# Kernel tuning notes

Hardware: AMD Instinct MI355X
Metric: run time of the kernel (lower is better)

The kernel has to match this reference:

```python
import jax, jax.numpy as jnp
import numpy as np

NUM_NODES = 100000
NUM_EDGES = 1600000
IN_DIM = 128
HID = 128
OUT_DIM = 5


def setup_inputs() -> dict:
    key = jax.random.key(0)
    ks = jax.random.split(key, 8)
    x = jax.random.normal(ks[0], (NUM_NODES, IN_DIM), dtype=jnp.float32)
    edges = jax.random.randint(ks[1], (2, NUM_EDGES), 0, NUM_NODES, dtype=jnp.int32)
    s = 1.0 / np.sqrt(IN_DIM)
    W1 = jax.random.uniform(ks[2], (IN_DIM, HID), jnp.float32, -s, s)
    b1 = jax.random.uniform(ks[3], (HID,), jnp.float32, -s, s)
    sh = 1.0 / np.sqrt(HID)
    W2 = jax.random.uniform(ks[4], (HID, HID), jnp.float32, -sh, sh)
    b2 = jax.random.uniform(ks[5], (HID,), jnp.float32, -sh, sh)
    Wp = jax.random.uniform(ks[6], (HID, OUT_DIM), jnp.float32, -sh, sh)
    bp = jax.random.uniform(ks[7], (OUT_DIM,), jnp.float32, -sh, sh)
    return {"x": x, "edges": edges, "W1": W1, "b1": b1, "W2": W2, "b2": b2, "Wp": Wp, "bp": bp}


def _gnn_layer(x, src, tgt, W, b):
    # scatter-add of source features into targets (mean aggregation)
    agg = jax.ops.segment_sum(x[src], tgt, num_segments=NUM_NODES)  # [N, d]
    cnt = jax.ops.segment_sum(jnp.ones_like(tgt, dtype=x.dtype), tgt, num_segments=NUM_NODES)
    cnt = jnp.maximum(cnt, 1.0)  # clamp(min=1)
    agg = agg / cnt[:, None]
    combined = x + agg  # residual
    return jax.nn.relu(combined @ W + b)


def reference(x, edges, W1, b1, W2, b2, Wp, bp):
    src, tgt = edges[0], edges[1]
    h = _gnn_layer(x, src, tgt, W1, b1)
    h = _gnn_layer(h, src, tgt, W2, b2)
    return h @ Wp + bp  # [N, OUT_DIM]
```

## Files before the change

### kernel.cpp

```cpp
#include <hip/hip_runtime.h>

typedef unsigned int uint32;
typedef unsigned short ushort16;

typedef __attribute__((ext_vector_type(8))) short short8;
typedef __attribute__((ext_vector_type(4))) float f32x4;


#define RSH 9
#define NRG 512
#define CAP 12288
#define CH  2048

__device__ __forceinline__ ushort16 f2bf(float f) {
    uint32 u = __float_as_uint(f);
    u += 0x7fffu + ((u >> 16) & 1u);
    return (ushort16)(u >> 16);
}
__device__ __forceinline__ float bfhi(uint32 u) { return __uint_as_float(u & 0xffff0000u); }
__device__ __forceinline__ float bflo(uint32 u) { return __uint_as_float(u << 16); }
__device__ __forceinline__ uint32 pack2(float a, float b) {
    return (uint32)f2bf(a) | ((uint32)f2bf(b) << 16);
}

union U16 { uint4 u; short8 s; };
__device__ __forceinline__ short8 ld_frag(const ushort16* p) {
    U16 x; x.u = *(const uint4*)p; return x.s;
}

#define ACC8(v) \
    acc[0] += bflo(v.x); acc[1] += bfhi(v.x); \
    acc[2] += bflo(v.y); acc[3] += bfhi(v.y); \
    acc[4] += bflo(v.z); acc[5] += bfhi(v.z); \
    acc[6] += bflo(v.w); acc[7] += bfhi(v.w);

__global__ __launch_bounds__(256)
void count_prep_kernel(const int* __restrict__ tgt, int* __restrict__ hist,
                       const float* __restrict__ W1, const float* __restrict__ W2,
                       ushort16* __restrict__ Wt1, ushort16* __restrict__ Wt2,
                       int E, int PB) {
    int tid = threadIdx.x, blk = blockIdx.x;
    if (blk >= PB) {
        int idx = blk - PB;
        const float* W = (idx >> 3) ? W2 : W1;
        ushort16* Wt = (idx >> 3) ? Wt2 : Wt1;
        int i0 = (idx & 7) * 2048 + tid * 8;
        float4 a = *(const float4*)(W + i0);
        float4 b = *(const float4*)(W + i0 + 4);
        int k = i0 >> 7, col = i0 & 127;
        Wt[(col + 0) * 128 + k] = f2bf(a.x);
        Wt[(col + 1) * 128 + k] = f2bf(a.y);
        Wt[(col + 2) * 128 + k] = f2bf(a.z);
        Wt[(col + 3) * 128 + k] = f2bf(a.w);
        Wt[(col + 4) * 128 + k] = f2bf(b.x);
        Wt[(col + 5) * 128 + k] = f2bf(b.y);
        Wt[(col + 6) * 128 + k] = f2bf(b.z);
        Wt[(col + 7) * 128 + k] = f2bf(b.w);
        return;
    }
    __shared__ int cnt[256];
    cnt[tid] = 0;
    __syncthreads();
    int q0 = blk * (CH / 4), q1 = min(q0 + CH / 4, E / 4);
    for (int q = q0 + tid; q < q1; q += 256) {
        int4 t = ((const int4*)tgt)[q];
        atomicAdd(&cnt[t.x >> RSH], 1);
        atomicAdd(&cnt[t.y >> RSH], 1);
        atomicAdd(&cnt[t.z >> RSH], 1);
        atomicAdd(&cnt[t.w >> RSH], 1);
    }
    if (blk == 0 && tid == 0)
        for (int e = (E / 4) * 4; e < E; ++e) atomicAdd(&cnt[tgt[e] >> RSH], 1);
    __syncthreads();
    hist[(size_t)blk * 256 + tid] = cnt[tid];
}

__global__ __launch_bounds__(256)
void scan_kernel(int* __restrict__ hist, int* __restrict__ total, int PB) {
    __shared__ int sd[256];
    __shared__ int carrySh;
    int r = blockIdx.x, tid = threadIdx.x;
    if (tid == 0) carrySh = 0;
    __syncthreads();
    int chunks = (PB + 255) >> 8;
    for (int ch = 0; ch < chunks; ++ch) {
        int g = ch * 256 + tid;
        int v = (g < PB) ? hist[(size_t)g * 256 + r] : 0;
        int c0 = carrySh;
        sd[tid] = v;
        __syncthreads();
        for (int o = 1; o < 256; o <<= 1) {
            int t = (tid >= o) ? sd[tid - o] : 0;
            __syncthreads();
            sd[tid] += t;
            __syncthreads();
        }
        if (g < PB) hist[(size_t)g * 256 + r] = sd[tid] - v + c0;
        int tot = sd[255];
        __syncthreads();
        if (tid == 0) carrySh = c0 + tot;
        __syncthreads();
    }
    if (tid == 0) total[r] = carrySh;
}

__global__ __launch_bounds__(256)
void scatter_kernel(const int* __restrict__ src, const int* __restrict__ tgt,
                    const int* __restrict__ hist, uint2* __restrict__ rlist,
                    int E) {
    __shared__ int cb[256];
    __shared__ int cnt[256];
    int tid = threadIdx.x, blk = blockIdx.x;
    cnt[tid] = 0;
    cb[tid] = hist[(size_t)blk * 256 + tid];
    __syncthreads();
    int q0 = blk * (CH / 4), q1 = min(q0 + CH / 4, E / 4);
    for (int q = q0 + tid; q < q1; q += 256) {
        int4 t = ((const int4*)tgt)[q];
        int4 s = ((const int4*)src)[q];
        int r0 = t.x >> RSH, r1 = t.y >> RSH, r2 = t.z >> RSH, r3 = t.w >> RSH;
        int p0 = cb[r0] + atomicAdd(&cnt[r0], 1);
        int p1 = cb[r1] + atomicAdd(&cnt[r1], 1);
        int p2 = cb[r2] + atomicAdd(&cnt[r2], 1);
        int p3 = cb[r3] + atomicAdd(&cnt[r3], 1);
        if (p0 < CAP) rlist[(size_t)r0 * CAP + p0] = make_uint2((uint32)s.x, (uint32)t.x);
        if (p1 < CAP) rlist[(size_t)r1 * CAP + p1] = make_uint2((uint32)s.y, (uint32)t.y);
        if (p2 < CAP) rlist[(size_t)r2 * CAP + p2] = make_uint2((uint32)s.z, (uint32)t.z);
        if (p3 < CAP) rlist[(size_t)r3 * CAP + p3] = make_uint2((uint32)s.w, (uint32)t.w);
    }
    if (blk == 0 && tid == 0) {
        for (int e = (E / 4) * 4; e < E; ++e) {
            int t = tgt[e], r = t >> RSH;
            int p = cb[r] + atomicAdd(&cnt[r], 1);
            if (p < CAP) rlist[(size_t)r * CAP + p] = make_uint2((uint32)src[e], (uint32)t);
        }
    }
}

__global__ __launch_bounds__(512)
void csr_cvt_kernel(const uint2* __restrict__ rlist, const int* __restrict__ total,
                    int* __restrict__ start, int* __restrict__ deg,
                    int* __restrict__ csr, int N, int R, int CVB,
                    const float* __restrict__ x, uint4* __restrict__ xb) {
    int blk = blockIdx.x;
    int tid = threadIdx.x;
    if (blk >= R) {
        int n16 = N * 16;
        for (int j = (blk - R) * 512 + tid; j < n16; j += CVB * 512) {
            const float* p = x + (size_t)j * 8;
            float4 a = *(const float4*)p;
            float4 b = *(const float4*)(p + 4);
            uint4 o;
            o.x = pack2(a.x, a.y); o.y = pack2(a.z, a.w);
            o.z = pack2(b.x, b.y); o.w = pack2(b.z, b.w);
            xb[j] = o;
        }
        return;
    }
    __shared__ int lhist[NRG];
    __shared__ int sd[512];
    __shared__ int rbaseSh, countSh;

    int r = blk;
    if (tid < 256) sd[tid] = (tid < R) ? total[tid] : 0;
    __syncthreads();
    for (int o = 1; o < 256; o <<= 1) {
        int t = (tid >= o && tid < 256) ? sd[tid - o] : 0;
        __syncthreads();
        if (tid < 256) sd[tid] += t;
        __syncthreads();
    }
    if (tid == 0) {
        rbaseSh = (r == 0) ? 0 : sd[r - 1];
        countSh = min(total[r], CAP);
    }
    if (tid < NRG) lhist[tid] = 0;
    __syncthreads();
    int count = countSh;
    const uint2* rl = rlist + (size_t)r * CAP;
    int n0 = r << RSH;

    {
        int i = tid;
        for (; i + 512 * 7 < count; i += 512 * 8) {
            uint2 e0 = rl[i], e1 = rl[i + 512], e2 = rl[i + 1024], e3 = rl[i + 1536];
            uint2 e4 = rl[i + 2048], e5 = rl[i + 2560], e6 = rl[i + 3072], e7 = rl[i + 3584];
            atomicAdd(&lhist[e0.y & (NRG - 1)], 1);
            atomicAdd(&lhist[e1.y & (NRG - 1)], 1);
            atomicAdd(&lhist[e2.y & (NRG - 1)], 1);
            atomicAdd(&lhist[e3.y & (NRG - 1)], 1);
            atomicAdd(&lhist[e4.y & (NRG - 1)], 1);
            atomicAdd(&lhist[e5.y & (NRG - 1)], 1);
            atomicAdd(&lhist[e6.y & (NRG - 1)], 1);
            atomicAdd(&lhist[e7.y & (NRG - 1)], 1);
        }
        for (; i < count; i += 512)
            atomicAdd(&lhist[rl[i].y & (NRG - 1)], 1);
    }
    __syncthreads();

    {
        int v = lhist[tid];
        sd[tid] = v;
        __syncthreads();
        for (int o = 1; o < 512; o <<= 1) {
            int t = (tid >= o) ? sd[tid - o] : 0;
            __syncthreads();
            sd[tid] += t;
            __syncthreads();
        }
        int excl = sd[tid] - v + rbaseSh;
        int node = n0 + tid;
        if (node < N) { start[node] = excl; deg[node] = v; }
        lhist[tid] = excl;
        __syncthreads();
    }

    {
        int i = tid;
        for (; i + 512 * 7 < count; i += 512 * 8) {
            uint2 e0 = rl[i], e1 = rl[i + 512], e2 = rl[i + 1024], e3 = rl[i + 1536];
            uint2 e4 = rl[i + 2048], e5 = rl[i + 2560], e6 = rl[i + 3072], e7 = rl[i + 3584];
            int p0 = atomicAdd(&lhist[e0.y & (NRG - 1)], 1);
            int p1 = atomicAdd(&lhist[e1.y & (NRG - 1)], 1);
            int p2 = atomicAdd(&lhist[e2.y & (NRG - 1)], 1);
            int p3 = atomicAdd(&lhist[e3.y & (NRG - 1)], 1);
            int p4 = atomicAdd(&lhist[e4.y & (NRG - 1)], 1);
            int p5 = atomicAdd(&lhist[e5.y & (NRG - 1)], 1);
            int p6 = atomicAdd(&lhist[e6.y & (NRG - 1)], 1);
            int p7 = atomicAdd(&lhist[e7.y & (NRG - 1)], 1);
            csr[p0] = (int)e0.x; csr[p1] = (int)e1.x;
            csr[p2] = (int)e2.x; csr[p3] = (int)e3.x;
            csr[p4] = (int)e4.x; csr[p5] = (int)e5.x;
            csr[p6] = (int)e6.x; csr[p7] = (int)e7.x;
        }
        for (; i < count; i += 512) {
            uint2 e = rl[i];
            int p = atomicAdd(&lhist[e.y & (NRG - 1)], 1);
            csr[p] = (int)e.x;
        }
    }
}

__global__ __launch_bounds__(256, 4)
void agg_combine_bf16_kernel(const ushort16* __restrict__ hb,
                             const int* __restrict__ startv, const int* __restrict__ degv,
                             const int* __restrict__ csr,
                             uint32* __restrict__ outb, int N) {
    int wid = (blockIdx.x * 256 + threadIdx.x) >> 6;
    int lane = threadIdx.x & 63;
    if (wid >= N) return;
    int g = lane >> 4, sl = lane & 15;
    int s0 = startv[wid];
    int deg = degv[wid];
    int fi = sl * 4 + g;
    uint32 su = ((const uint32*)hb)[(size_t)wid * 64 + fi];

    float acc[8];
#pragma unroll
    for (int j = 0; j < 8; ++j) acc[j] = 0.f;

    int base = 0;
    for (; base + 8 <= deg; base += 8) {
        int i0 = csr[s0 + base + g];
        int i1 = csr[s0 + base + 4 + g];
        uint4 v0 = *(const uint4*)(hb + (size_t)i0 * 128 + sl * 8);
        uint4 v1 = *(const uint4*)(hb + (size_t)i1 * 128 + sl * 8);
        ACC8(v0); ACC8(v1);
    }
    for (; base < deg; base += 4) {
        int e = base + g;
        if (e < deg) {
            int s = csr[s0 + e];
            uint4 v = *(const uint4*)(hb + (size_t)s * 128 + sl * 8);
            ACC8(v);
        }
    }
#pragma unroll
    for (int j = 0; j < 8; ++j) {
        acc[j] += __shfl_xor(acc[j], 16, 64);
        acc[j] += __shfl_xor(acc[j], 32, 64);
    }
    float inv = 1.f / fmaxf((float)deg, 1.f);
    float ax = (g == 0) ? acc[0] : (g == 1) ? acc[2] : (g == 2) ? acc[4] : acc[6];
    float ay = (g == 0) ? acc[1] : (g == 1) ? acc[3] : (g == 2) ? acc[5] : acc[7];
    outb[(size_t)wid * 64 + fi] = pack2(bflo(su) + ax * inv, bfhi(su) + ay * inv);
}

__global__ __launch_bounds__(256)
void gemm_mfma_kernel(const ushort16* __restrict__ A, const ushort16* __restrict__ Wt,
                      const float* __restrict__ bias, int M,
                      ushort16* __restrict__ outB,
                      const float* __restrict__ Wp, const float* __restrict__ bp,
                      float* __restrict__ outP) {
    const int tid = threadIdx.x;
    const int lane = tid & 63;
    const int wave = tid >> 6;
    const int l15 = lane & 15;
    const int quad = lane >> 4;
    const int r0 = blockIdx.x * 64 + wave * 16;

    int arow = r0 + l15;
    if (arow >= M) arow = M - 1;
    const ushort16* aptr = A + (size_t)arow * 128 + quad * 8;
    short8 afr[4];
#pragma unroll
    for (int kt = 0; kt < 4; ++kt) afr[kt] = ld_frag(aptr + kt * 32);

    f32x4 acc[8];
#pragma unroll
    for (int t = 0; t < 8; ++t) acc[t] = (f32x4){0.f, 0.f, 0.f, 0.f};

#pragma unroll
    for (int t = 0; t < 8; ++t) {
        const ushort16* bptr = Wt + (size_t)(16 * t + l15) * 128 + quad * 8;
        short8 b0 = ld_frag(bptr);
        short8 b1 = ld_frag(bptr + 32);
        short8 b2 = ld_frag(bptr + 64);
        short8 b3 = ld_frag(bptr + 96);
        acc[t] = __builtin_amdgcn_mfma_f32_16x16x32_bf16(afr[0], b0, acc[t], 0, 0, 0);
        acc[t] = __builtin_amdgcn_mfma_f32_16x16x32_bf16(afr[1], b1, acc[t], 0, 0, 0);
        acc[t] = __builtin_amdgcn_mfma_f32_16x16x32_bf16(afr[2], b2, acc[t], 0, 0, 0);
        acc[t] = __builtin_amdgcn_mfma_f32_16x16x32_bf16(afr[3], b3, acc[t], 0, 0, 0);
    }

    if (outP) {
        float p[4][5];
#pragma unroll
        for (int r = 0; r < 4; ++r)
#pragma unroll
            for (int j = 0; j < 5; ++j) p[r][j] = 0.f;
#pragma unroll
        for (int t = 0; t < 8; ++t) {
            float wpl[5];
#pragma unroll
            for (int j = 0; j < 5; ++j) wpl[j] = Wp[(16 * t + l15) * 5 + j];
            float bt = bias[16 * t + l15];
            float ov[4];
            ov[0] = fmaxf(acc[t].x + bt, 0.f);
            ov[1] = fmaxf(acc[t].y + bt, 0.f);
            ov[2] = fmaxf(acc[t].z + bt, 0.f);
            ov[3] = fmaxf(acc[t].w + bt, 0.f);
#pragma unroll
            for (int r = 0; r < 4; ++r)
#pragma unroll
                for (int j = 0; j < 5; ++j) p[r][j] += ov[r] * wpl[j];
        }
#pragma unroll
        for (int m = 1; m <= 8; m <<= 1)
#pragma unroll
            for (int r = 0; r < 4; ++r)
#pragma unroll
                for (int j = 0; j < 5; ++j) p[r][j] += __shfl_xor(p[r][j], m, 64);
        if (l15 == 0) {
#pragma unroll
            for (int r = 0; r < 4; ++r) {
                int row = r0 + quad * 4 + r;
                if (row < M) {
#pragma unroll
                    for (int j = 0; j < 5; ++j) outP[(size_t)row * 5 + j] = p[r][j] + bp[j];
                }
            }
        }
    } else {
#pragma unroll
        for (int t = 0; t < 8; ++t) {
            float bt = bias[16 * t + l15];
            float ov[4];
            ov[0] = fmaxf(acc[t].x + bt, 0.f);
            ov[1] = fmaxf(acc[t].y + bt, 0.f);
            ov[2] = fmaxf(acc[t].z + bt, 0.f);
            ov[3] = fmaxf(acc[t].w + bt, 0.f);
#pragma unroll
            for (int r = 0; r < 4; ++r) {
                float nb = __shfl_xor(ov[r], 1, 64);
                int row = r0 + quad * 4 + r;
                if (((l15 & 1) == 0) && row < M) {
                    *(uint32*)(outB + (size_t)row * 128 + 16 * t + l15) = pack2(ov[r], nb);
                }
            }
        }
    }
}

extern "C" void kernel_launch(void* const* d_in, const int* in_sizes, int n_in,
                              void* d_out, int out_size, void* d_ws, size_t ws_size,
                              hipStream_t stream) {
    const float* x     = (const float*)d_in[0];
    const int*   edges = (const int*)d_in[1];
    const float* W1    = (const float*)d_in[2];
    const float* b1    = (const float*)d_in[3];
    const float* W2    = (const float*)d_in[4];
    const float* b2    = (const float*)d_in[5];
    const float* Wp    = (const float*)d_in[6];
    const float* bp    = (const float*)d_in[7];
    float* out = (float*)d_out;

    int N = in_sizes[0] / 128;
    int E = in_sizes[1] / 2;
    const int* src = edges;
    const int* tgt = edges + E;

    const int R  = (N + NRG - 1) >> RSH;
    const int PB = (E + CH - 1) / CH;
    const int CVB = 304;

    char* ws = (char*)d_ws;
    size_t off = 0;
    auto alloc = [&](size_t bytes) {
        char* p = ws + off;
        off = (off + bytes + 255) & ~(size_t)255;
        return p;
    };
    int*      deg     = (int*)alloc((size_t)N * 4);
    int*      start   = (int*)alloc((size_t)N * 4);
    int*      csr     = (int*)alloc((size_t)E * 4);
    int*      hist    = (int*)alloc((size_t)PB * 256 * 4);
    int*      total   = (int*)alloc(256 * 4);
    ushort16* xb      = (ushort16*)alloc((size_t)N * 128 * 2);
    ushort16* hb1     = (ushort16*)alloc((size_t)N * 128 * 2);
    ushort16* bufAb   = (ushort16*)alloc((size_t)N * 128 * 2);
    ushort16* Wt1     = (ushort16*)alloc(128 * 128 * 2);
    ushort16* Wt2     = (ushort16*)alloc(128 * 128 * 2);
    uint2*    rlist   = (uint2*)bufAb;
    (void)ws_size;

    const int gemmBlocks = (N + 63) / 64;
    const int aggBlocks  = (N + 3) / 4;

    count_prep_kernel<<<PB + 16, 256, 0, stream>>>(tgt, hist, W1, W2, Wt1, Wt2, E, PB);
    scan_kernel<<<R, 256, 0, stream>>>(hist, total, PB);
    scatter_kernel<<<PB, 256, 0, stream>>>(src, tgt, hist, rlist, E);
    csr_cvt_kernel<<<R + CVB, 512, 0, stream>>>(rlist, total, start, deg, csr,
                                                N, R, CVB, x, (uint4*)xb);
    agg_combine_bf16_kernel<<<aggBlocks, 256, 0, stream>>>(xb, start, deg, csr,
                                                           (uint32*)bufAb, N);
    gemm_mfma_kernel<<<gemmBlocks, 256, 0, stream>>>(bufAb, Wt1, b1, N, hb1,
                                                     nullptr, nullptr, nullptr);
    agg_combine_bf16_kernel<<<aggBlocks, 256, 0, stream>>>(hb1, start, deg, csr,
                                                           (uint32*)bufAb, N);
    gemm_mfma_kernel<<<gemmBlocks, 256, 0, stream>>>(bufAb, Wt2, b2, N, nullptr,
                                                     Wp, bp, out);
}
```

Measured before the change: 332.5 us.

## Reorder GNN layers as transform-then-aggregate and fuse the final projection into aggregation

Each layer now applies the linear transform before mean aggregation, relying on linearity: (x+agg(x))W = xW + agg(xW). The first GEMM reads fp32 x directly inside the CSR-build kernel, and the second GEMM fuses layer-1 bias+ReLU into its A-load. The final layer aggregates the transformed features, then applies bias, ReLU and the 5-wide projection in the same pass, which removes a separate x-to-bf16 conversion kernel and the last GEMM. The histogram and scatter kernels use 1024-thread blocks over larger chunks so the scan becomes a single pass. The cost is different bf16 rounding points and an rlist buffer that is now allocated separately instead of aliasing another buffer.

```diff
diff --git a/kernel.cpp b/kernel.cpp
--- a/kernel.cpp
+++ b/kernel.cpp
@@ -10,7 +10,7 @@
 #define RSH 9
 #define NRG 512
 #define CAP 12288
-#define CH  2048
+#define CH2 16384
 
 __device__ __forceinline__ ushort16 f2bf(float f) {
     uint32 u = __float_as_uint(f);
@@ -34,35 +34,26 @@
     acc[4] += bflo(v.z); acc[5] += bfhi(v.z); \
     acc[6] += bflo(v.w); acc[7] += bfhi(v.w);
 
-__global__ __launch_bounds__(256)
+__global__ __launch_bounds__(1024)
 void count_prep_kernel(const int* __restrict__ tgt, int* __restrict__ hist,
                        const float* __restrict__ W1, const float* __restrict__ W2,
                        ushort16* __restrict__ Wt1, ushort16* __restrict__ Wt2,
                        int E, int PB) {
     int tid = threadIdx.x, blk = blockIdx.x;
     if (blk >= PB) {
-        int idx = blk - PB;
-        const float* W = (idx >> 3) ? W2 : W1;
-        ushort16* Wt = (idx >> 3) ? Wt2 : Wt1;
-        int i0 = (idx & 7) * 2048 + tid * 8;
-        float4 a = *(const float4*)(W + i0);
-        float4 b = *(const float4*)(W + i0 + 4);
-        int k = i0 >> 7, col = i0 & 127;
-        Wt[(col + 0) * 128 + k] = f2bf(a.x);
-        Wt[(col + 1) * 128 + k] = f2bf(a.y);
-        Wt[(col + 2) * 128 + k] = f2bf(a.z);
-        Wt[(col + 3) * 128 + k] = f2bf(a.w);
-        Wt[(col + 4) * 128 + k] = f2bf(b.x);
-        Wt[(col + 5) * 128 + k] = f2bf(b.y);
-        Wt[(col + 6) * 128 + k] = f2bf(b.z);
-        Wt[(col + 7) * 128 + k] = f2bf(b.w);
+        const float* W = (blk - PB) ? W2 : W1;
+        ushort16* Wt = (blk - PB) ? Wt2 : Wt1;
+        for (int i = tid; i < 16384; i += 1024) {
+            int k = i >> 7, c = i & 127;
+            Wt[c * 128 + k] = f2bf(W[i]);
+        }
         return;
     }
     __shared__ int cnt[256];
-    cnt[tid] = 0;
-    __syncthreads();
-    int q0 = blk * (CH / 4), q1 = min(q0 + CH / 4, E / 4);
-    for (int q = q0 + tid; q < q1; q += 256) {
+    if (tid < 256) cnt[tid] = 0;
+    __syncthreads();
+    int q0 = blk * (CH2 / 4), q1 = min(q0 + CH2 / 4, E / 4);
+    for (int q = q0 + tid; q < q1; q += 1024) {
         int4 t = ((const int4*)tgt)[q];
         atomicAdd(&cnt[t.x >> RSH], 1);
         atomicAdd(&cnt[t.y >> RSH], 1);
@@ -72,50 +63,40 @@
     if (blk == 0 && tid == 0)
         for (int e = (E / 4) * 4; e < E; ++e) atomicAdd(&cnt[tgt[e] >> RSH], 1);
     __syncthreads();
-    hist[(size_t)blk * 256 + tid] = cnt[tid];
+    if (tid < 256) hist[(size_t)blk * 256 + tid] = cnt[tid];
 }
 
 __global__ __launch_bounds__(256)
 void scan_kernel(int* __restrict__ hist, int* __restrict__ total, int PB) {
     __shared__ int sd[256];
-    __shared__ int carrySh;
     int r = blockIdx.x, tid = threadIdx.x;
-    if (tid == 0) carrySh = 0;
-    __syncthreads();
-    int chunks = (PB + 255) >> 8;
-    for (int ch = 0; ch < chunks; ++ch) {
-        int g = ch * 256 + tid;
-        int v = (g < PB) ? hist[(size_t)g * 256 + r] : 0;
-        int c0 = carrySh;
-        sd[tid] = v;
-        __syncthreads();
-        for (int o = 1; o < 256; o <<= 1) {
-            int t = (tid >= o) ? sd[tid - o] : 0;
-            __syncthreads();
-            sd[tid] += t;
-            __syncthreads();
-        }
-        if (g < PB) hist[(size_t)g * 256 + r] = sd[tid] - v + c0;
-        int tot = sd[255];
-        __syncthreads();
-        if (tid == 0) carrySh = c0 + tot;
-        __syncthreads();
-    }
-    if (tid == 0) total[r] = carrySh;
-}
-
-__global__ __launch_bounds__(256)
+    int v = (tid < PB) ? hist[(size_t)tid * 256 + r] : 0;
+    sd[tid] = v;
+    __syncthreads();
+    for (int o = 1; o < 256; o <<= 1) {
+        int t = (tid >= o) ? sd[tid - o] : 0;
+        __syncthreads();
+        sd[tid] += t;
+        __syncthreads();
+    }
+    if (tid < PB) hist[(size_t)tid * 256 + r] = sd[tid] - v;
+    if (tid == 255) total[r] = sd[255];
+}
+
+__global__ __launch_bounds__(1024)
 void scatter_kernel(const int* __restrict__ src, const int* __restrict__ tgt,
                     const int* __restrict__ hist, uint2* __restrict__ rlist,
                     int E) {
     __shared__ int cb[256];
     __shared__ int cnt[256];
     int tid = threadIdx.x, blk = blockIdx.x;
-    cnt[tid] = 0;
-    cb[tid] = hist[(size_t)blk * 256 + tid];
-    __syncthreads();
-    int q0 = blk * (CH / 4), q1 = min(q0 + CH / 4, E / 4);
-    for (int q = q0 + tid; q < q1; q += 256) {
+    if (tid < 256) {
+        cnt[tid] = 0;
+        cb[tid] = hist[(size_t)blk * 256 + tid];
+    }
+    __syncthreads();
+    int q0 = blk * (CH2 / 4), q1 = min(q0 + CH2 / 4, E / 4);
+    for (int q = q0 + tid; q < q1; q += 1024) {
         int4 t = ((const int4*)tgt)[q];
         int4 s = ((const int4*)src)[q];
         int r0 = t.x >> RSH, r1 = t.y >> RSH, r2 = t.z >> RSH, r3 = t.w >> RSH;
@@ -137,24 +118,96 @@
     }
 }
 
+template<int MODE>
+__device__ __forceinline__
+void gemm_rows(const void* __restrict__ Asrc, const ushort16* __restrict__ Wt,
+               const float* __restrict__ bias, int M,
+               ushort16* __restrict__ outB, int r0w) {
+    const int lane = threadIdx.x & 63;
+    const int l15 = lane & 15;
+    const int quad = lane >> 4;
+
+    int arow = r0w + l15;
+    if (arow >= M) arow = M - 1;
+
+    short8 afr[4];
+    if (MODE == 1) {
+        const float* ap = (const float*)Asrc + (size_t)arow * 128 + quad * 8;
+#pragma unroll
+        for (int kt = 0; kt < 4; ++kt) {
+            float4 a0 = *(const float4*)(ap + kt * 32);
+            float4 a1 = *(const float4*)(ap + kt * 32 + 4);
+            short8 f;
+            f[0] = (short)f2bf(a0.x); f[1] = (short)f2bf(a0.y);
+            f[2] = (short)f2bf(a0.z); f[3] = (short)f2bf(a0.w);
+            f[4] = (short)f2bf(a1.x); f[5] = (short)f2bf(a1.y);
+            f[6] = (short)f2bf(a1.z); f[7] = (short)f2bf(a1.w);
+            afr[kt] = f;
+        }
+    } else if (MODE == 2) {
+        const ushort16* aptr = (const ushort16*)Asrc + (size_t)arow * 128 + quad * 8;
+#pragma unroll
+        for (int kt = 0; kt < 4; ++kt) {
+            uint4 v = *(const uint4*)(aptr + kt * 32);
+            const float* bb = bias + kt * 32 + quad * 8;
+            float4 b0 = *(const float4*)bb;
+            float4 b1 = *(const float4*)(bb + 4);
+            uint32 w0 = pack2(fmaxf(bflo(v.x) + b0.x, 0.f), fmaxf(bfhi(v.x) + b0.y, 0.f));
+            uint32 w1 = pack2(fmaxf(bflo(v.y) + b0.z, 0.f), fmaxf(bfhi(v.y) + b0.w, 0.f));
+            uint32 w2 = pack2(fmaxf(bflo(v.z) + b1.x, 0.f), fmaxf(bfhi(v.z) + b1.y, 0.f));
+            uint32 w3 = pack2(fmaxf(bflo(v.w) + b1.z, 0.f), fmaxf(bfhi(v.w) + b1.w, 0.f));
+            U16 u; u.u = make_uint4(w0, w1, w2, w3);
+            afr[kt] = u.s;
+        }
+    } else {
+        const ushort16* aptr = (const ushort16*)Asrc + (size_t)arow * 128 + quad * 8;
+#pragma unroll
+        for (int kt = 0; kt < 4; ++kt) afr[kt] = ld_frag(aptr + kt * 32);
+    }
+
+    f32x4 acc[8];
+#pragma unroll
+    for (int t = 0; t < 8; ++t) acc[t] = (f32x4){0.f, 0.f, 0.f, 0.f};
+
+#pragma unroll
+    for (int t = 0; t < 8; ++t) {
+        const ushort16* bptr = Wt + (size_t)(16 * t + l15) * 128 + quad * 8;
+        short8 b0 = ld_frag(bptr);
+        short8 b1 = ld_frag(bptr + 32);
+        short8 b2 = ld_frag(bptr + 64);
+        short8 b3 = ld_frag(bptr + 96);
+        acc[t] = __builtin_amdgcn_mfma_f32_16x16x32_bf16(afr[0], b0, acc[t], 0, 0, 0);
+        acc[t] = __builtin_amdgcn_mfma_f32_16x16x32_bf16(afr[1], b1, acc[t], 0, 0, 0);
+        acc[t] = __builtin_amdgcn_mfma_f32_16x16x32_bf16(afr[2], b2, acc[t], 0, 0, 0);
+        acc[t] = __builtin_amdgcn_mfma_f32_16x16x32_bf16(afr[3], b3, acc[t], 0, 0, 0);
+    }
+
+#pragma unroll
+    for (int t = 0; t < 8; ++t) {
+        float ov[4];
+        ov[0] = acc[t].x; ov[1] = acc[t].y; ov[2] = acc[t].z; ov[3] = acc[t].w;
+#pragma unroll
+        for (int r = 0; r < 4; ++r) {
+            float nb = __shfl_xor(ov[r], 1, 64);
+            int row = r0w + quad * 4 + r;
+            if (((l15 & 1) == 0) && row < M) {
+                *(uint32*)(outB + (size_t)row * 128 + 16 * t + l15) = pack2(ov[r], nb);
+            }
+        }
+    }
+}
+
 __global__ __launch_bounds__(512)
-void csr_cvt_kernel(const uint2* __restrict__ rlist, const int* __restrict__ total,
-                    int* __restrict__ start, int* __restrict__ deg,
-                    int* __restrict__ csr, int N, int R, int CVB,
-                    const float* __restrict__ x, uint4* __restrict__ xb) {
+void csr_gemm1_kernel(const uint2* __restrict__ rlist, const int* __restrict__ total,
+                      int* __restrict__ start, int* __restrict__ deg,
+                      int* __restrict__ csr, int N, int R,
+                      const float* __restrict__ x, const ushort16* __restrict__ Wt1,
+                      ushort16* __restrict__ ybuf) {
     int blk = blockIdx.x;
     int tid = threadIdx.x;
     if (blk >= R) {
-        int n16 = N * 16;
-        for (int j = (blk - R) * 512 + tid; j < n16; j += CVB * 512) {
-            const float* p = x + (size_t)j * 8;
-            float4 a = *(const float4*)p;
-            float4 b = *(const float4*)(p + 4);
-            uint4 o;
-            o.x = pack2(a.x, a.y); o.y = pack2(a.z, a.w);
-            o.z = pack2(b.x, b.y); o.w = pack2(b.z, b.w);
-            xb[j] = o;
-        }
+        int gid = blk - R;
+        gemm_rows<1>(x, Wt1, nullptr, N, ybuf, gid * 128 + (tid >> 6) * 16);
         return;
     }
     __shared__ int lhist[NRG];
@@ -242,6 +295,13 @@
     }
 }
 
+__global__ __launch_bounds__(256)
+void gemm_biasrelu_kernel(const ushort16* __restrict__ A, const ushort16* __restrict__ Wt,
+                          const float* __restrict__ bias, int M,
+                          ushort16* __restrict__ outB) {
+    gemm_rows<2>(A, Wt, bias, M, outB, blockIdx.x * 64 + ((threadIdx.x >> 6)) * 16);
+}
+
 __global__ __launch_bounds__(256, 4)
 void agg_combine_bf16_kernel(const ushort16* __restrict__ hb,
                              const int* __restrict__ startv, const int* __restrict__ degv,
@@ -287,99 +347,65 @@
     outb[(size_t)wid * 64 + fi] = pack2(bflo(su) + ax * inv, bfhi(su) + ay * inv);
 }
 
-__global__ __launch_bounds__(256)
-void gemm_mfma_kernel(const ushort16* __restrict__ A, const ushort16* __restrict__ Wt,
-                      const float* __restrict__ bias, int M,
-                      ushort16* __restrict__ outB,
-                      const float* __restrict__ Wp, const float* __restrict__ bp,
-                      float* __restrict__ outP) {
-    const int tid = threadIdx.x;
-    const int lane = tid & 63;
-    const int wave = tid >> 6;
-    const int l15 = lane & 15;
-    const int quad = lane >> 4;
-    const int r0 = blockIdx.x * 64 + wave * 16;
-
-    int arow = r0 + l15;
-    if (arow >= M) arow = M - 1;
-    const ushort16* aptr = A + (size_t)arow * 128 + quad * 8;
-    short8 afr[4];
-#pragma unroll
-    for (int kt = 0; kt < 4; ++kt) afr[kt] = ld_frag(aptr + kt * 32);
-
-    f32x4 acc[8];
-#pragma unroll
-    for (int t = 0; t < 8; ++t) acc[t] = (f32x4){0.f, 0.f, 0.f, 0.f};
-
-#pragma unroll
-    for (int t = 0; t < 8; ++t) {
-        const ushort16* bptr = Wt + (size_t)(16 * t + l15) * 128 + quad * 8;
-        short8 b0 = ld_frag(bptr);
-        short8 b1 = ld_frag(bptr + 32);
-        short8 b2 = ld_frag(bptr + 64);
-        short8 b3 = ld_frag(bptr + 96);
-        acc[t] = __builtin_amdgcn_mfma_f32_16x16x32_bf16(afr[0], b0, acc[t], 0, 0, 0);
-        acc[t] = __builtin_amdgcn_mfma_f32_16x16x32_bf16(afr[1], b1, acc[t], 0, 0, 0);
-        acc[t] = __builtin_amdgcn_mfma_f32_16x16x32_bf16(afr[2], b2, acc[t], 0, 0, 0);
-        acc[t] = __builtin_amdgcn_mfma_f32_16x16x32_bf16(afr[3], b3, acc[t], 0, 0, 0);
-    }
-
-    if (outP) {
-        float p[4][5];
-#pragma unroll
-        for (int r = 0; r < 4; ++r)
-#pragma unroll
-            for (int j = 0; j < 5; ++j) p[r][j] = 0.f;
-#pragma unroll
-        for (int t = 0; t < 8; ++t) {
-            float wpl[5];
-#pragma unroll
-            for (int j = 0; j < 5; ++j) wpl[j] = Wp[(16 * t + l15) * 5 + j];
-            float bt = bias[16 * t + l15];
-            float ov[4];
-            ov[0] = fmaxf(acc[t].x + bt, 0.f);
-            ov[1] = fmaxf(acc[t].y + bt, 0.f);
-            ov[2] = fmaxf(acc[t].z + bt, 0.f);
-            ov[3] = fmaxf(acc[t].w + bt, 0.f);
-#pragma unroll
-            for (int r = 0; r < 4; ++r)
-#pragma unroll
-                for (int j = 0; j < 5; ++j) p[r][j] += ov[r] * wpl[j];
-        }
-#pragma unroll
-        for (int m = 1; m <= 8; m <<= 1)
-#pragma unroll
-            for (int r = 0; r < 4; ++r)
-#pragma unroll
-                for (int j = 0; j < 5; ++j) p[r][j] += __shfl_xor(p[r][j], m, 64);
-        if (l15 == 0) {
-#pragma unroll
-            for (int r = 0; r < 4; ++r) {
-                int row = r0 + quad * 4 + r;
-                if (row < M) {
-#pragma unroll
-                    for (int j = 0; j < 5; ++j) outP[(size_t)row * 5 + j] = p[r][j] + bp[j];
-                }
-            }
-        }
-    } else {
-#pragma unroll
-        for (int t = 0; t < 8; ++t) {
-            float bt = bias[16 * t + l15];
-            float ov[4];
-            ov[0] = fmaxf(acc[t].x + bt, 0.f);
-            ov[1] = fmaxf(acc[t].y + bt, 0.f);
-            ov[2] = fmaxf(acc[t].z + bt, 0.f);
-            ov[3] = fmaxf(acc[t].w + bt, 0.f);
-#pragma unroll
-            for (int r = 0; r < 4; ++r) {
-                float nb = __shfl_xor(ov[r], 1, 64);
-                int row = r0 + quad * 4 + r;
-                if (((l15 & 1) == 0) && row < M) {
-                    *(uint32*)(outB + (size_t)row * 128 + 16 * t + l15) = pack2(ov[r], nb);
-                }
-            }
-        }
+__global__ __launch_bounds__(256, 4)
+void agg_proj_kernel(const ushort16* __restrict__ hb,
+                     const int* __restrict__ startv, const int* __restrict__ degv,
+                     const int* __restrict__ csr,
+                     const float* __restrict__ bias,
+                     const float* __restrict__ Wp, const float* __restrict__ bp,
+                     float* __restrict__ outP, int N) {
+    int wid = (blockIdx.x * 256 + threadIdx.x) >> 6;
+    int lane = threadIdx.x & 63;
+    if (wid >= N) return;
+    int g = lane >> 4, sl = lane & 15;
+    int s0 = startv[wid];
+    int deg = degv[wid];
+    int fi = sl * 4 + g;
+    uint32 su = ((const uint32*)hb)[(size_t)wid * 64 + fi];
+
+    float acc[8];
+#pragma unroll
+    for (int j = 0; j < 8; ++j) acc[j] = 0.f;
+
+    int base = 0;
+    for (; base + 8 <= deg; base += 8) {
+        int i0 = csr[s0 + base + g];
+        int i1 = csr[s0 + base + 4 + g];
+        uint4 v0 = *(const uint4*)(hb + (size_t)i0 * 128 + sl * 8);
+        uint4 v1 = *(const uint4*)(hb + (size_t)i1 * 128 + sl * 8);
+        ACC8(v0); ACC8(v1);
+    }
+    for (; base < deg; base += 4) {
+        int e = base + g;
+        if (e < deg) {
+            int s = csr[s0 + e];
+            uint4 v = *(const uint4*)(hb + (size_t)s * 128 + sl * 8);
+            ACC8(v);
+        }
+    }
+#pragma unroll
+    for (int j = 0; j < 8; ++j) {
+        acc[j] += __shfl_xor(acc[j], 16, 64);
+        acc[j] += __shfl_xor(acc[j], 32, 64);
+    }
+    float inv = 1.f / fmaxf((float)deg, 1.f);
+    float ax = (g == 0) ? acc[0] : (g == 1) ? acc[2] : (g == 2) ? acc[4] : acc[6];
+    float ay = (g == 0) ? acc[1] : (g == 1) ? acc[3] : (g == 2) ? acc[5] : acc[7];
+
+    float ha = fmaxf(bflo(su) + ax * inv + bias[2 * fi],     0.f);
+    float hc = fmaxf(bfhi(su) + ay * inv + bias[2 * fi + 1], 0.f);
+
+    float p[5];
+#pragma unroll
+    for (int j = 0; j < 5; ++j)
+        p[j] = ha * Wp[(2 * fi) * 5 + j] + hc * Wp[(2 * fi + 1) * 5 + j];
+#pragma unroll
+    for (int m = 1; m <= 32; m <<= 1)
+#pragma unroll
+        for (int j = 0; j < 5; ++j) p[j] += __shfl_xor(p[j], m, 64);
+    if (lane == 0) {
+#pragma unroll
+        for (int j = 0; j < 5; ++j) outP[(size_t)wid * 5 + j] = p[j] + bp[j];
     }
 }
 
@@ -402,8 +428,7 @@
     const int* tgt = edges + E;
 
     const int R  = (N + NRG - 1) >> RSH;
-    const int PB = (E + CH - 1) / CH;
-    const int CVB = 304;
+    const int PB = (E + CH2 - 1) / CH2;
 
     char* ws = (char*)d_ws;
     size_t off = 0;
@@ -417,28 +442,25 @@
     int*      csr     = (int*)alloc((size_t)E * 4);
     int*      hist    = (int*)alloc((size_t)PB * 256 * 4);
     int*      total   = (int*)alloc(256 * 4);
-    ushort16* xb      = (ushort16*)alloc((size_t)N * 128 * 2);
-    ushort16* hb1     = (ushort16*)alloc((size_t)N * 128 * 2);
-    ushort16* bufAb   = (ushort16*)alloc((size_t)N * 128 * 2);
+    uint2*    rlist   = (uint2*)alloc((size_t)R * CAP * 8);
+    ushort16* ybuf    = (ushort16*)alloc((size_t)N * 128 * 2);
+    ushort16* abuf    = (ushort16*)alloc((size_t)N * 128 * 2);
     ushort16* Wt1     = (ushort16*)alloc(128 * 128 * 2);
     ushort16* Wt2     = (ushort16*)alloc(128 * 128 * 2);
-    uint2*    rlist   = (uint2*)bufAb;
     (void)ws_size;
 
+    const int g1Blocks   = (N + 127) / 128;
     const int gemmBlocks = (N + 63) / 64;
     const int aggBlocks  = (N + 3) / 4;
 
-    count_prep_kernel<<<PB + 16, 256, 0, stream>>>(tgt, hist, W1, W2, Wt1, Wt2, E, PB);
+    count_prep_kernel<<<PB + 2, 1024, 0, stream>>>(tgt, hist, W1, W2, Wt1, Wt2, E, PB);
     scan_kernel<<<R, 256, 0, stream>>>(hist, total, PB);
-    scatter_kernel<<<PB, 256, 0, stream>>>(src, tgt, hist, rlist, E);
-    csr_cvt_kernel<<<R + CVB, 512, 0, stream>>>(rlist, total, start, deg, csr,
-                                                N, R, CVB, x, (uint4*)xb);
-    agg_combine_bf16_kernel<<<aggBlocks, 256, 0, stream>>>(xb, start, deg, csr,
-                                                           (uint32*)bufAb, N);
-    gemm_mfma_kernel<<<gemmBlocks, 256, 0, stream>>>(bufAb, Wt1, b1, N, hb1,
-                                                     nullptr, nullptr, nullptr);
-    agg_combine_bf16_kernel<<<aggBlocks, 256, 0, stream>>>(hb1, start, deg, csr,
-                                                           (uint32*)bufAb, N);
-    gemm_mfma_kernel<<<gemmBlocks, 256, 0, stream>>>(bufAb, Wt2, b2, N, nullptr,
-                                                     Wp, bp, out);
-}
+    scatter_kernel<<<PB, 1024, 0, stream>>>(src, tgt, hist, rlist, E);
+    csr_gemm1_kernel<<<R + g1Blocks, 512, 0, stream>>>(rlist, total, start, deg,
+                                                       csr, N, R, x, Wt1, ybuf);
+    agg_combine_bf16_kernel<<<aggBlocks, 256, 0, stream>>>(ybuf, start, deg, csr,
+                                                           (uint32*)abuf, N);
+    gemm_biasrelu_kernel<<<gemmBlocks, 256, 0, stream>>>(abuf, Wt2, b1, N, ybuf);
+    agg_proj_kernel<<<aggBlocks, 256, 0, stream>>>(ybuf, start, deg, csr, b2,
+                                                   Wp, bp, out, N);
+}
```

Result: no change. 334.6 us (+0.6%).
